# Optimization experiments

Measured on AMD Instinct MI355X. Metric: run time of the kernel, lower is better.

The kernel has to match this reference:

```python
import jax, jax.numpy as jnp
import numpy as np

N, E, DIN, H, HEADS = 50000, 800000, 128, 64, 4


def setup_inputs() -> dict:
    key = jax.random.key(0)
    ks = jax.random.split(key, 12)

    def p(k, shape, fan_in):
        return jax.random.normal(k, shape, dtype=jnp.float32) / np.float32(np.sqrt(fan_in))

    return dict(
        x=jax.random.normal(ks[0], (N, DIN), dtype=jnp.float32),
        edge_index=jax.random.randint(ks[1], (2, E), 0, N, dtype=jnp.int32),
        # GCNConv(input_dim, hidden)
        W_gcn=p(ks[2], (DIN, H), DIN), b_gcn=jnp.zeros((H,), jnp.float32),
        # GATConv(hidden, hidden, heads=4, concat=True)
        W_gat=p(ks[3], (H, HEADS * H), H),
        att_src=p(ks[4], (HEADS, H), H), att_dst=p(ks[5], (HEADS, H), H),
        b_gat=jnp.zeros((HEADS * H,), jnp.float32),
        # SAGEConv(4*hidden, hidden): lin_l (neighbors, with bias), lin_r (root, no bias)
        W_sage_l=p(ks[6], (HEADS * H, H), HEADS * H), b_sage=jnp.zeros((H,), jnp.float32),
        W_sage_r=p(ks[7], (HEADS * H, H), HEADS * H),
        # edge-pair MLP: Linear(2*hidden, hidden) -> ReLU -> Linear(hidden, 1)
        W1=p(ks[8], (2 * H, H), 2 * H), b1=jnp.zeros((H,), jnp.float32),
        W2=p(ks[9], (H, 1), H), b2=jnp.zeros((1,), jnp.float32),
    )


def reference(x, edge_index, W_gcn, b_gcn, W_gat, att_src, att_dst, b_gat,
              W_sage_l, b_sage, W_sage_r, W1, b1, W2, b2):
    n = x.shape[0]
    src, dst = edge_index[0], edge_index[1]
    loop = jnp.arange(n, dtype=edge_index.dtype)
    # edges with self-loops appended (GCN and GAT add self-loops by default)
    s2 = jnp.concatenate([src, loop])
    d2 = jnp.concatenate([dst, loop])

    h = x @ W_gcn                                            # [N, H]
    deg = jax.ops.segment_sum(jnp.ones_like(d2, jnp.float32), d2, num_segments=n)
    dinv = jnp.where(deg > 0, jax.lax.rsqrt(jnp.maximum(deg, 1e-12)), 0.0)
    norm = dinv[s2] * dinv[d2]                               # [E+N]
    h = jax.ops.segment_sum(h[s2] * norm[:, None], d2, num_segments=n) + b_gcn
    h = jax.nn.relu(h)                                       # dropout: identity in eval

    # ---- GATConv (heads=4, concat=True, negative_slope=0.2) ----
    g = (h @ W_gat).reshape(n, HEADS, H)                     # [N, heads, C]
    a_s = jnp.sum(g * att_src, axis=-1)                      # [N, heads]
    a_d = jnp.sum(g * att_dst, axis=-1)
    e = jax.nn.leaky_relu(a_s[s2] + a_d[d2], 0.2)            # [E+N, heads]
    m = jax.ops.segment_max(e, d2, num_segments=n)           # per-target max (stable softmax)
    e = jnp.exp(e - m[d2])
    z = jax.ops.segment_sum(e, d2, num_segments=n)
    alpha = e / (z[d2] + 1e-16)                              # edge softmax over incoming edges
    g = jax.ops.segment_sum(g[s2] * alpha[:, :, None], d2, num_segments=n)
    g = jax.nn.relu(g.reshape(n, HEADS * H) + b_gat)

    # ---- SAGEConv (mean aggregation, root weight, no self-loops) ----
    nsum = jax.ops.segment_sum(g[src], dst, num_segments=n)
    cnt = jax.ops.segment_sum(jnp.ones_like(dst, jnp.float32), dst, num_segments=n)
    mean = nsum / jnp.maximum(cnt, 1.0)[:, None]
    s = jax.nn.relu(mean @ W_sage_l + b_sage + g @ W_sage_r)  # [N, H]

    # ---- edge-pair MLP + sigmoid ----
    ef = jnp.concatenate([s[src], s[dst]], axis=1)            # [E, 2H]
    pred = jax.nn.relu(ef @ W1 + b1) @ W2 + b2                # [E, 1]
    return jax.nn.sigmoid(pred[:, 0])
```

## Files before the change

kernel.cpp:

```cpp
#include <hip/hip_runtime.h>
#include <math.h>

typedef float v2f __attribute__((ext_vector_type(2)));
static __device__ __forceinline__ float4 f4s(float v){ return make_float4(v,v,v,v); }
static __device__ __forceinline__ float4 f4add(float4 a, float4 b){ return make_float4(a.x+b.x,a.y+b.y,a.z+b.z,a.w+b.w); }
static __device__ __forceinline__ float4 f4max(float4 a, float4 b){ return make_float4(fmaxf(a.x,b.x),fmaxf(a.y,b.y),fmaxf(a.z,b.z),fmaxf(a.w,b.w)); }
static __device__ __forceinline__ float4 f4scale(float4 a, float s){ return make_float4(a.x*s,a.y*s,a.z*s,a.w*s); }
static __device__ __forceinline__ float4 f4fma(float4 acc, float s, float4 b){
  acc.x += s*b.x; acc.y += s*b.y; acc.z += s*b.z; acc.w += s*b.w; return acc;
}
static __device__ __forceinline__ float4 f4relu(float4 a){ return f4max(a, f4s(0.f)); }
static __device__ __forceinline__ float4 f4leaky(float4 a){
  return make_float4(a.x>0.f?a.x:0.2f*a.x, a.y>0.f?a.y:0.2f*a.y, a.z>0.f?a.z:0.2f*a.z, a.w>0.f?a.w:0.2f*a.w);
}
static __device__ __forceinline__ float4 f4expf(float4 a){ return make_float4(__expf(a.x),__expf(a.y),__expf(a.z),__expf(a.w)); }
static __device__ __forceinline__ unsigned short f2bf(float f){
  unsigned int u = __float_as_uint(f);
  unsigned int r = (u + 0x7fffu + ((u >> 16) & 1u)) >> 16;
  return (unsigned short)r;
}
static __device__ __forceinline__ ushort4 f2bf4(float4 f){
  ushort4 r; r.x=f2bf(f.x); r.y=f2bf(f.y); r.z=f2bf(f.z); r.w=f2bf(f.w); return r;
}
static __device__ __forceinline__ float4 bfu2f4(uint2 u){
  return make_float4(__uint_as_float(u.x << 16), __uint_as_float(u.x & 0xffff0000u),
                     __uint_as_float(u.y << 16), __uint_as_float(u.y & 0xffff0000u));
}
static __device__ __forceinline__ float4 bfu2f4_lo(uint4 u){ return bfu2f4(make_uint2(u.x, u.y)); }
static __device__ __forceinline__ float4 bfu2f4_hi(uint4 u){ return bfu2f4(make_uint2(u.z, u.w)); }

typedef __attribute__((ext_vector_type(8))) unsigned short u16x8;
static __device__ __forceinline__ u16x8 f2bf8(float4 a, float4 b){
  u16x8 r;
  r[0]=f2bf(a.x); r[1]=f2bf(a.y); r[2]=f2bf(a.z); r[3]=f2bf(a.w);
  r[4]=f2bf(b.x); r[5]=f2bf(b.y); r[6]=f2bf(b.z); r[7]=f2bf(b.w);
  return r;
}
static __device__ __forceinline__ void red2(float4& a, float4& b){
  a.x += __shfl_xor(a.x, 8); a.y += __shfl_xor(a.y, 8);
  a.z += __shfl_xor(a.z, 8); a.w += __shfl_xor(a.w, 8);
  b.x += __shfl_xor(b.x, 8); b.y += __shfl_xor(b.y, 8);
  b.z += __shfl_xor(b.z, 8); b.w += __shfl_xor(b.w, 8);
}
static __device__ __forceinline__ unsigned char f2fp8(float v){
  return (unsigned char)(__builtin_amdgcn_cvt_pk_fp8_f32(v, v, 0, false) & 0xff);
}
static __device__ __forceinline__ unsigned int f4_fp8x4(float4 v){
  unsigned int r = __builtin_amdgcn_cvt_pk_fp8_f32(v.x, v.y, 0, false);
  r = __builtin_amdgcn_cvt_pk_fp8_f32(v.z, v.w, r, true);
  return r;
}
static __device__ __forceinline__ float4 fp8x4_f4(unsigned int q){
  v2f lo = __builtin_amdgcn_cvt_pk_f32_fp8(q, false);
  v2f hi = __builtin_amdgcn_cvt_pk_f32_fp8(q, true);
  return make_float4(lo[0], lo[1], hi[0], hi[1]);
}

typedef __attribute__((ext_vector_type(8))) short bf16x8;
typedef __attribute__((ext_vector_type(4))) float f32x4;

__global__ __launch_bounds__(256) void k_rank(const int* __restrict__ dst, int* __restrict__ cnt,
                                              int* __restrict__ rank, int E){
  int t = blockIdx.x*256 + threadIdx.x;
  if (t < E) rank[t] = atomicAdd(&cnt[dst[t]], 1);
}
__global__ __launch_bounds__(256) void k_scan1(const int* __restrict__ cnt, int* __restrict__ excl,
                                               int* __restrict__ bsum, int n){
  __shared__ int sc[256];
  int t = threadIdx.x; int i = blockIdx.x*256 + t;
  int v = (i<n)?cnt[i]:0;
  sc[t]=v; __syncthreads();
  for (int o=1;o<256;o<<=1){ int a=(t>=o)?sc[t-o]:0; __syncthreads(); sc[t]+=a; __syncthreads(); }
  if (i<n) excl[i] = sc[t]-v;
  if (t==255) bsum[blockIdx.x] = sc[t];
}
__global__ __launch_bounds__(256) void k_scan2v(int* __restrict__ bsum, int nb,
                                                const float* __restrict__ Wg, const float* __restrict__ as,
                                                const float* __restrict__ ad, float* __restrict__ Vs,
                                                float* __restrict__ Vd){
  __shared__ int sc[256];
  int t = threadIdx.x;
  int v = (t<nb)?bsum[t]:0;
  sc[t]=v; __syncthreads();
  for (int o=1;o<256;o<<=1){ int a=(t>=o)?sc[t-o]:0; __syncthreads(); sc[t]+=a; __syncthreads(); }
  if (t<nb) bsum[t] = sc[t]-v;
  int h = t >> 6, k = t & 63;
  float s = 0.f, d = 0.f;
  const float* wr = Wg + (size_t)k*256 + h*64;
  const float* ar = as + h*64;
  const float* dr = ad + h*64;
  for (int c = 0; c < 64; ++c){ float w = wr[c]; s += w*ar[c]; d += w*dr[c]; }
  Vs[t] = s; Vd[t] = d;
}
__global__ __launch_bounds__(256) void k_scan3(const int* __restrict__ cnt, const int* __restrict__ excl,
                                               const int* __restrict__ bsum, int* __restrict__ offs,
                                               float* __restrict__ dinv, int n, int E){
  int i = blockIdx.x*256 + threadIdx.x;
  if (i < n){
    int o = excl[i] + bsum[blockIdx.x];
    offs[i] = o;
    dinv[i] = rsqrtf((float)cnt[i] + 1.0f);
    if (i == 0) offs[n] = E;
  }
}
__global__ __launch_bounds__(256) void k_fill(const int* __restrict__ src, const int* __restrict__ dst,
                                              const int* __restrict__ offs, const int* __restrict__ rank,
                                              int* __restrict__ csr, int E){
  int t = blockIdx.x*256 + threadIdx.x;
  if (t < E) csr[offs[dst[t]] + rank[t]] = src[t];
}

__global__ __launch_bounds__(256) void k_asdh(const unsigned short* __restrict__ Hh,
                                              const float* __restrict__ Vs, const float* __restrict__ Vd,
                                              float* __restrict__ D, int n){
  __shared__ float vs[256], vd[256];
  int t = threadIdx.x;
  vs[t] = Vs[t]; vd[t] = Vd[t];
  __syncthreads();
  int idx = blockIdx.x*256 + t;
  if (idx >= n*4) return;
  int nd = idx >> 2, h = idx & 3;
  const unsigned short* hr = Hh + (size_t)nd*64;
  const float* vsr = vs + h*64;
  const float* vdr = vd + h*64;
  float s = 0.f, d = 0.f;
  #pragma unroll
  for (int k = 0; k < 8; ++k){
    uint4 u = *(const uint4*)(hr + k*8);
    float4 lo = bfu2f4_lo(u), hi = bfu2f4_hi(u);
    const float* a = vsr + k*8;
    const float* b = vdr + k*8;
    s += lo.x*a[0]+lo.y*a[1]+lo.z*a[2]+lo.w*a[3] + hi.x*a[4]+hi.y*a[5]+hi.z*a[6]+hi.w*a[7];
    d += lo.x*b[0]+lo.y*b[1]+lo.z*b[2]+lo.w*b[3] + hi.x*b[4]+hi.y*b[5]+hi.z*b[6]+hi.w*b[7];
  }
  D[(size_t)nd*8 + h]     = s;
  D[(size_t)nd*8 + 4 + h] = d;
}

template<int K, int Cout, bool IBF16, bool SCALE, bool DUAL, bool H4, bool BRELU, bool OB16, bool O8>
__global__ __launch_bounds__(256) void k_mgemm(const void* __restrict__ in, int ldin,
                                               const float* __restrict__ Wa, int ldwa,
                                               const float* __restrict__ Wb, int ldwb,
                                               unsigned short* __restrict__ out,
                                               unsigned char* __restrict__ out8, int ldout,
                                               int n, const float* __restrict__ rowscale,
                                               const float* __restrict__ bias){
  constexpr int CC = Cout >> 4;
  constexpr int KB = K >> 5;
  constexpr int NH = H4 ? 4 : 1;
  extern __shared__ unsigned short wb[];
  int tid = threadIdx.x;
  constexpr int nslots = KB*CC*64;
  for (int s = tid; s < nslots; s += 256){
    int l = s & 63;
    int f = s >> 6;
    int cc = f % CC, kb = f / CC;
    int c  = cc*16 + (l & 15);
    int kr = kb*32 + ((l >> 4) << 3);
    const float* wp; int ld;
    if (DUAL && c >= (Cout/2)){ wp = Wb + (size_t)kr*ldwb + (c - Cout/2); ld = ldwb; }
    else                      { wp = Wa + (size_t)kr*ldwa + c;            ld = ldwa; }
    unsigned short* dp = &wb[s*8];
    #pragma unroll
    for (int j = 0; j < 8; ++j) dp[j] = f2bf(wp[(size_t)j*ld]);
  }
  __syncthreads();
  int wv = tid >> 6, l = tid & 63;
  int lrow = l & 15;
  int lk = (l >> 4) << 3;
  int ngrp = (n + 63) >> 6;
  const unsigned short* inb = (const unsigned short*)in;
  const float* inf = (const float*)in;
  for (int g = blockIdx.x; g < ngrp; g += gridDim.x){
    int r0 = (g << 6) + (wv << 4);
    int m = r0 + lrow;
    bf16x8 afr[NH][KB];
    #pragma unroll
    for (int h = 0; h < NH; ++h){
      #pragma unroll
      for (int kb = 0; kb < KB; ++kb){
        bf16x8 a = {0,0,0,0,0,0,0,0};
        if (m < n){
          int off = (H4 ? h*64 : 0) + kb*32 + lk;
          if (IBF16){
            a = *(const bf16x8*)(inb + (size_t)m*ldin + off);
          } else {
            const float* p = inf + (size_t)m*ldin + off;
            float4 f0 = *(const float4*)p;
            float4 f1 = *(const float4*)(p + 4);
            a[0]=(short)f2bf(f0.x); a[1]=(short)f2bf(f0.y); a[2]=(short)f2bf(f0.z); a[3]=(short)f2bf(f0.w);
            a[4]=(short)f2bf(f1.x); a[5]=(short)f2bf(f1.y); a[6]=(short)f2bf(f1.z); a[7]=(short)f2bf(f1.w);
          }
        }
        afr[h][kb] = a;
      }
    }
    int rbase = r0 + ((l >> 4) << 2);
    float sc[4];
    if (SCALE){
      #pragma unroll
      for (int r = 0; r < 4; ++r) sc[r] = (rbase + r < n) ? rowscale[rbase + r] : 0.f;
    }
    #pragma unroll
    for (int cc = 0; cc < CC; ++cc){
      f32x4 acc = {0.f, 0.f, 0.f, 0.f};
      constexpr int hstep = H4 ? 1 : 0;
      int hh = hstep ? (cc >> 2) : 0;
      #pragma unroll
      for (int kb = 0; kb < KB; ++kb){
        bf16x8 b = *(const bf16x8*)&wb[((kb*CC + cc)*64 + l)*8];
        acc = __builtin_amdgcn_mfma_f32_16x16x32_bf16(afr[hh][kb], b, acc, 0, 0, 0);
      }
      int c = cc*16 + lrow;
      float bv = BRELU ? bias[c] : 0.f;
      #pragma unroll
      for (int r = 0; r < 4; ++r){
        int rr = rbase + r;
        if (rr < n){
          float v = acc[r];
          if (SCALE) v *= sc[r];
          if (BRELU) v = fmaxf(v + bv, 0.f);
          if (OB16) out[(size_t)rr*ldout + c] = f2bf(v);
          if (O8)   out8[(size_t)rr*ldout + c] = f2fp8(v);
        }
      }
    }
  }
}

__global__ __launch_bounds__(256) void k_gcn(const unsigned char* __restrict__ a8, const float* __restrict__ dinv,
                                             const float* __restrict__ b, const int* __restrict__ offs,
                                             const int* __restrict__ csr, unsigned short* __restrict__ h,
                                             unsigned char* __restrict__ h8, int n){
  int l = threadIdx.x & 63;
  int node = (((blockIdx.x*256 + threadIdx.x) >> 6) << 2) + (l >> 4);
  int l15 = l & 15;
  int grp = l15 >> 3, sub = l15 & 7;
  bool ok = node < n;
  int beg = 0, end = 0;
  float di = 0.f;
  if (ok){ beg = offs[node]; end = offs[node+1]; di = dinv[node]; }
  float4 aL0 = f4s(0.f), aH0 = f4s(0.f), aL1 = f4s(0.f), aH1 = f4s(0.f);
  int i = beg + grp;
  for (; i + 2 < end; i += 4){
    int s0 = csr[i], s1 = csr[i+2];
    uint2 u0 = *(const uint2*)(a8 + (size_t)s0*64 + (sub<<3));
    uint2 u1 = *(const uint2*)(a8 + (size_t)s1*64 + (sub<<3));
    aL0 = f4add(aL0, fp8x4_f4(u0.x)); aH0 = f4add(aH0, fp8x4_f4(u0.y));
    aL1 = f4add(aL1, fp8x4_f4(u1.x)); aH1 = f4add(aH1, fp8x4_f4(u1.y));
  }
  if (i < end){
    int s0 = csr[i];
    uint2 u0 = *(const uint2*)(a8 + (size_t)s0*64 + (sub<<3));
    aL0 = f4add(aL0, fp8x4_f4(u0.x)); aH0 = f4add(aH0, fp8x4_f4(u0.y));
  }
  float4 aL = f4add(aL0, aL1), aH = f4add(aH0, aH1);
  red2(aL, aH);
  if (ok && grp == 0){
    uint2 us = *(const uint2*)(a8 + (size_t)node*64 + (sub<<3));
    aL = f4add(aL, fp8x4_f4(us.x)); aH = f4add(aH, fp8x4_f4(us.y));
    float4 b0 = *(const float4*)(b + (sub<<3));
    float4 b1 = *(const float4*)(b + (sub<<3) + 4);
    float4 r0 = f4relu(f4fma(b0, di, aL));
    float4 r1 = f4relu(f4fma(b1, di, aH));
    *(u16x8*)(h + (size_t)node*64 + (sub<<3)) = f2bf8(r0, r1);
    uint2 q; q.x = f4_fp8x4(r0); q.y = f4_fp8x4(r1);
    *(uint2*)(h8 + (size_t)node*64 + (sub<<3)) = q;
  }
}

#define GAT_CAP 128
__global__ __launch_bounds__(256) void k_gat2(const float* __restrict__ D, const unsigned char* __restrict__ H8,
                                              const int* __restrict__ offs, const int* __restrict__ csr,
                                              unsigned short* __restrict__ Y, int n){
  __shared__ float wl[8][GAT_CAP*4];
  __shared__ int   sl[8][GAT_CAP];
  int hw = threadIdx.x >> 5;
  int node = (blockIdx.x*256 + threadIdx.x) >> 5;
  int l5 = threadIdx.x & 31;
  if (node >= n) return;
  int beg = offs[node], end = offs[node+1];
  int deg = end - beg;
  float4 ed  = *(const float4*)(D + (size_t)node*8 + 4);
  float4 es0 = *(const float4*)(D + (size_t)node*8);
  float4 wself = f4expf(f4leaky(f4add(es0, ed)));
  float4 z4 = f4s(0.f);
  for (int i = beg + l5; i < end; i += 32){
    int s = csr[i];
    float4 w = f4expf(f4leaky(f4add(*(const float4*)(D + (size_t)s*8), ed)));
    int li = i - beg;
    if (li < GAT_CAP){ *(float4*)&wl[hw][li<<2] = w; sl[hw][li] = s << 6; }
    z4 = f4add(z4, w);
  }
  for (int m = 1; m < 32; m <<= 1){
    z4.x += __shfl_xor(z4.x, m); z4.y += __shfl_xor(z4.y, m);
    z4.z += __shfl_xor(z4.z, m); z4.w += __shfl_xor(z4.w, m);
  }
  z4 = f4add(z4, wself);
  int grp = l5 >> 4;
  int sub = l5 & 15;
  int c0b = sub << 2;
  float4 a0 = f4s(0.f), a1 = f4s(0.f), a2 = f4s(0.f), a3 = f4s(0.f);
  int nl = deg < GAT_CAP ? deg : GAT_CAP;
  int i = grp;
  for (; i + 2 < nl; i += 4){
    int o0 = sl[hw][i], o1 = sl[hw][i+2];
    float4 w0 = *(const float4*)&wl[hw][i<<2];
    float4 w1 = *(const float4*)&wl[hw][(i+2)<<2];
    unsigned int q0 = *(const unsigned int*)(H8 + o0 + c0b);
    unsigned int q1 = *(const unsigned int*)(H8 + o1 + c0b);
    float4 f0 = fp8x4_f4(q0);
    float4 f1 = fp8x4_f4(q1);
    a0 = f4fma(a0, w0.x, f0); a1 = f4fma(a1, w0.y, f0);
    a2 = f4fma(a2, w0.z, f0); a3 = f4fma(a3, w0.w, f0);
    a0 = f4fma(a0, w1.x, f1); a1 = f4fma(a1, w1.y, f1);
    a2 = f4fma(a2, w1.z, f1); a3 = f4fma(a3, w1.w, f1);
  }
  if (i < nl){
    float4 w0 = *(const float4*)&wl[hw][i<<2];
    float4 f0 = fp8x4_f4(*(const unsigned int*)(H8 + sl[hw][i] + c0b));
    a0 = f4fma(a0, w0.x, f0); a1 = f4fma(a1, w0.y, f0);
    a2 = f4fma(a2, w0.z, f0); a3 = f4fma(a3, w0.w, f0);
  }
  for (int j = nl + grp; j < deg; j += 2){
    int s = csr[beg+j];
    float4 e = f4leaky(f4add(*(const float4*)(D + (size_t)s*8), ed));
    float4 w = f4expf(e);
    float4 f0 = fp8x4_f4(*(const unsigned int*)(H8 + ((size_t)s << 6) + c0b));
    a0 = f4fma(a0, w.x, f0); a1 = f4fma(a1, w.y, f0);
    a2 = f4fma(a2, w.z, f0); a3 = f4fma(a3, w.w, f0);
  }
  a0.x += __shfl_xor(a0.x, 16); a0.y += __shfl_xor(a0.y, 16); a0.z += __shfl_xor(a0.z, 16); a0.w += __shfl_xor(a0.w, 16);
  a1.x += __shfl_xor(a1.x, 16); a1.y += __shfl_xor(a1.y, 16); a1.z += __shfl_xor(a1.z, 16); a1.w += __shfl_xor(a1.w, 16);
  a2.x += __shfl_xor(a2.x, 16); a2.y += __shfl_xor(a2.y, 16); a2.z += __shfl_xor(a2.z, 16); a2.w += __shfl_xor(a2.w, 16);
  a3.x += __shfl_xor(a3.x, 16); a3.y += __shfl_xor(a3.y, 16); a3.z += __shfl_xor(a3.z, 16); a3.w += __shfl_xor(a3.w, 16);
  if (grp == 0){
    float4 fs = fp8x4_f4(*(const unsigned int*)(H8 + ((size_t)node << 6) + c0b));
    a0 = f4fma(a0, wself.x, fs);
    a1 = f4fma(a1, wself.y, fs);
    a2 = f4fma(a2, wself.z, fs);
    a3 = f4fma(a3, wself.w, fs);
    a0 = f4scale(a0, 1.f/(z4.x + 1e-16f));
    a1 = f4scale(a1, 1.f/(z4.y + 1e-16f));
    a2 = f4scale(a2, 1.f/(z4.z + 1e-16f));
    a3 = f4scale(a3, 1.f/(z4.w + 1e-16f));
    unsigned short* yp = Y + (size_t)node*256 + (sub << 2);
    *(ushort4*)(yp)       = f2bf4(a0);
    *(ushort4*)(yp + 64)  = f2bf4(a1);
    *(ushort4*)(yp + 128) = f2bf4(a2);
    *(ushort4*)(yp + 192) = f2bf4(a3);
  }
}

__global__ __launch_bounds__(256) void k_sage(const unsigned char* __restrict__ T8, const unsigned short* __restrict__ T,
                                              const float* __restrict__ b, const int* __restrict__ offs,
                                              const int* __restrict__ csr, unsigned short* __restrict__ S, int n){
  int l = threadIdx.x & 63;
  int node = (((blockIdx.x*256 + threadIdx.x) >> 6) << 2) + (l >> 4);
  int l15 = l & 15;
  int grp = l15 >> 3, sub = l15 & 7;
  bool ok = node < n;
  int beg = 0, end = 0;
  if (ok){ beg = offs[node]; end = offs[node+1]; }
  float4 aL0 = f4s(0.f), aH0 = f4s(0.f), aL1 = f4s(0.f), aH1 = f4s(0.f);
  int i = beg + grp;
  for (; i + 2 < end; i += 4){
    int s0 = csr[i], s1 = csr[i+2];
    uint2 u0 = *(const uint2*)(T8 + (size_t)s0*128 + (sub<<3));
    uint2 u1 = *(const uint2*)(T8 + (size_t)s1*128 + (sub<<3));
    aL0 = f4add(aL0, fp8x4_f4(u0.x)); aH0 = f4add(aH0, fp8x4_f4(u0.y));
    aL1 = f4add(aL1, fp8x4_f4(u1.x)); aH1 = f4add(aH1, fp8x4_f4(u1.y));
  }
  if (i < end){
    int s0 = csr[i];
    uint2 u0 = *(const uint2*)(T8 + (size_t)s0*128 + (sub<<3));
    aL0 = f4add(aL0, fp8x4_f4(u0.x)); aH0 = f4add(aH0, fp8x4_f4(u0.y));
  }
  float4 aL = f4add(aL0, aL1), aH = f4add(aH0, aH1);
  red2(aL, aH);
  if (ok && grp == 0){
    float minv = 1.f / fmaxf((float)(end - beg), 1.f);
    uint4 ur = *(const uint4*)(T + (size_t)node*128 + 64 + (sub<<3));
    float4 b0 = *(const float4*)(b + (sub<<3));
    float4 b1 = *(const float4*)(b + (sub<<3) + 4);
    float4 r0 = f4relu(f4add(f4fma(b0, minv, aL), bfu2f4_lo(ur)));
    float4 r1 = f4relu(f4add(f4fma(b1, minv, aH), bfu2f4_hi(ur)));
    *(u16x8*)(S + (size_t)node*64 + (sub<<3)) = f2bf8(r0, r1);
  }
}

__global__ __launch_bounds__(256) void k_mlp(const unsigned char* __restrict__ T2,
                                             const float* __restrict__ b1, const float* __restrict__ W2,
                                             const float* __restrict__ b2, const int* __restrict__ src,
                                             const int* __restrict__ dst, float* __restrict__ out, int E){
  int t = threadIdx.x;
  int e = blockIdx.x*32 + (t >> 3);
  if (e >= E) return;
  int sub = t & 7;
  int s = src[e], d = dst[e];
  uint2 uu = *(const uint2*)(T2 + (size_t)s*128 + (sub<<3));
  uint2 vv = *(const uint2*)(T2 + (size_t)d*128 + 64 + (sub<<3));
  float4 u0 = fp8x4_f4(uu.x), u1 = fp8x4_f4(uu.y);
  float4 v0 = fp8x4_f4(vv.x), v1 = fp8x4_f4(vv.y);
  float4 bb0 = *(const float4*)(b1 + (sub<<3));
  float4 bb1 = *(const float4*)(b1 + (sub<<3) + 4);
  float4 w0 = *(const float4*)(W2 + (sub<<3));
  float4 w1 = *(const float4*)(W2 + (sub<<3) + 4);
  float4 ta = f4relu(f4add(f4add(u0, v0), bb0));
  float4 tb = f4relu(f4add(f4add(u1, v1), bb1));
  float p = ta.x*w0.x + ta.y*w0.y + ta.z*w0.z + ta.w*w0.w
          + tb.x*w1.x + tb.y*w1.y + tb.z*w1.z + tb.w*w1.w;
  p += __shfl_xor(p, 1);
  p += __shfl_xor(p, 2);
  p += __shfl_xor(p, 4);
  if (sub == 0) out[e] = 1.f / (1.f + __expf(-(p + b2[0])));
}

extern "C" void kernel_launch(void* const* d_in, const int* in_sizes, int n_in,
                              void* d_out, int out_size, void* d_ws, size_t ws_size,
                              hipStream_t stream){
  const float* x     = (const float*)d_in[0];
  const int*   eidx  = (const int*)  d_in[1];
  const float* W_gcn = (const float*)d_in[2];
  const float* b_gcn = (const float*)d_in[3];
  const float* W_gat = (const float*)d_in[4];
  const float* att_s = (const float*)d_in[5];
  const float* att_d = (const float*)d_in[6];
  const float* b_gat = (const float*)d_in[7];
  const float* W_sl  = (const float*)d_in[8];
  const float* b_sg  = (const float*)d_in[9];
  const float* W_sr  = (const float*)d_in[10];
  const float* W1    = (const float*)d_in[11];
  const float* b1    = (const float*)d_in[12];
  const float* W2    = (const float*)d_in[13];
  const float* b2    = (const float*)d_in[14];
  float* out = (float*)d_out;

  const int N = in_sizes[0] / 128;
  const int E = in_sizes[1] / 2;
  const int* src = eidx;
  const int* dst = eidx + E;

  float* ws   = (float*)d_ws;
  float* dinv = ws;
  float* D    = dinv + (size_t)N;
  float* Vs   = D + (size_t)N*8;
  float* Vd   = Vs + 256;
  unsigned short* A0 = (unsigned short*)(Vd + 256);
  unsigned short* H  = A0 + (size_t)N*64;
  unsigned short* Y  = H  + (size_t)N*64;
  unsigned short* G  = Y  + (size_t)N*256;
  unsigned short* T  = G  + (size_t)N*256;
  unsigned short* S  = T  + (size_t)N*128;
  unsigned char*  A8 = (unsigned char*)(S + (size_t)N*64);
  unsigned char*  H8 = A8 + (size_t)N*64;
  unsigned char*  T8 = H8 + (size_t)N*64;
  unsigned char*  T2 = T8 + (size_t)N*128;
  int* cnt  = (int*)(T2 + (size_t)N*128);
  int* excl = cnt + N;
  int* bsum = excl + N;
  int* offs = bsum + 256;
  int* rank = offs + N + 1;
  int* csr  = rank + E;

  const int nb = (N + 255) / 256;
  const int gtiles = (N + 63) / 64;
  const int nwb = (N + 15) / 16;

  hipMemsetAsync(cnt, 0, (size_t)N*sizeof(int), stream);
  k_rank<<<(E+255)/256, 256, 0, stream>>>(dst, cnt, rank, E);
  k_scan1<<<nb, 256, 0, stream>>>(cnt, excl, bsum, N);
  k_scan2v<<<1, 256, 0, stream>>>(bsum, nb, W_gat, att_s, att_d, Vs, Vd);
  k_scan3<<<nb, 256, 0, stream>>>(cnt, excl, bsum, offs, dinv, N, E);
  k_fill<<<(E+255)/256, 256, 0, stream>>>(src, dst, offs, rank, csr, E);

  k_mgemm<128, 64, false, true, false, false, false, false, true><<<gtiles, 256, 128*64*2, stream>>>(
      x, 128, W_gcn, 64, nullptr, 0, nullptr, A8, 64, N, dinv, nullptr);
  k_gcn <<<nwb, 256, 0, stream>>>(A8, dinv, b_gcn, offs, csr, H, H8, N);
  k_asdh<<<(N*4+255)/256, 256, 0, stream>>>(H, Vs, Vd, D, N);

  k_gat2<<<(N+7)/8, 256, 0, stream>>>(D, H8, offs, csr, Y, N);
  k_mgemm<64, 256, true, false, false, true, true, true, false><<<gtiles, 256, 64*256*2, stream>>>(
      Y, 256, W_gat, 256, nullptr, 0, G, nullptr, 256, N, nullptr, b_gat);

  k_mgemm<256, 128, true, false, true, false, false, true, true><<<gtiles, 256, 256*128*2, stream>>>(
      G, 256, W_sl, 64, W_sr, 64, T, T8, 128, N, nullptr, nullptr);
  k_sage<<<nwb, 256, 0, stream>>>(T8, T, b_sg, offs, csr, S, N);

  k_mgemm<64, 128, true, false, true, false, false, false, true><<<gtiles, 256, 64*128*2, stream>>>(
      S, 64, W1, 64, W1 + 64*64, 64, nullptr, T2, 128, N, nullptr, nullptr);
  k_mlp <<<(E+31)/32, 256, 0, stream>>>(T2, b1, W2, b2, src, dst, out, E);
}
```

Baseline: 323.2 us.

## Fuse GAT and SAGE GEMMs into one persistent kernel; fold attention dots into GCN

The two back-to-back GEMMs (GAT output projection with bias and ReLU, then the SAGE dual projection) become one persistent kernel. It keeps the intermediate 256-wide G tile in LDS instead of writing and re-reading it from global memory, and stages both weight matrices once per block. The per-node attention dot products (the former k_asdh) move into the GCN aggregation kernel, which removes a launch and the bf16 H buffer. SAGE now reads only the 64-wide fp8 neighbour projection and a separate bf16 root buffer. The cost is a large LDS footprint that limits occupancy, and a fixed grid of 256 blocks.

```diff
diff --git a/kernel.cpp b/kernel.cpp
--- a/kernel.cpp
+++ b/kernel.cpp
@@ -54,6 +54,9 @@
   v2f lo = __builtin_amdgcn_cvt_pk_f32_fp8(q, false);
   v2f hi = __builtin_amdgcn_cvt_pk_f32_fp8(q, true);
   return make_float4(lo[0], lo[1], hi[0], hi[1]);
+}
+static __device__ __forceinline__ float dot8(float4 a, float4 b, const float* v){
+  return a.x*v[0]+a.y*v[1]+a.z*v[2]+a.w*v[3]+b.x*v[4]+b.y*v[5]+b.z*v[6]+b.w*v[7];
 }
 
 typedef __attribute__((ext_vector_type(8))) short bf16x8;
@@ -108,33 +111,6 @@
                                               int* __restrict__ csr, int E){
   int t = blockIdx.x*256 + threadIdx.x;
   if (t < E) csr[offs[dst[t]] + rank[t]] = src[t];
-}
-
-__global__ __launch_bounds__(256) void k_asdh(const unsigned short* __restrict__ Hh,
-                                              const float* __restrict__ Vs, const float* __restrict__ Vd,
-                                              float* __restrict__ D, int n){
-  __shared__ float vs[256], vd[256];
-  int t = threadIdx.x;
-  vs[t] = Vs[t]; vd[t] = Vd[t];
-  __syncthreads();
-  int idx = blockIdx.x*256 + t;
-  if (idx >= n*4) return;
-  int nd = idx >> 2, h = idx & 3;
-  const unsigned short* hr = Hh + (size_t)nd*64;
-  const float* vsr = vs + h*64;
-  const float* vdr = vd + h*64;
-  float s = 0.f, d = 0.f;
-  #pragma unroll
-  for (int k = 0; k < 8; ++k){
-    uint4 u = *(const uint4*)(hr + k*8);
-    float4 lo = bfu2f4_lo(u), hi = bfu2f4_hi(u);
-    const float* a = vsr + k*8;
-    const float* b = vdr + k*8;
-    s += lo.x*a[0]+lo.y*a[1]+lo.z*a[2]+lo.w*a[3] + hi.x*a[4]+hi.y*a[5]+hi.z*a[6]+hi.w*a[7];
-    d += lo.x*b[0]+lo.y*b[1]+lo.z*b[2]+lo.w*b[3] + hi.x*b[4]+hi.y*b[5]+hi.z*b[6]+hi.w*b[7];
-  }
-  D[(size_t)nd*8 + h]     = s;
-  D[(size_t)nd*8 + 4 + h] = d;
 }
 
 template<int K, int Cout, bool IBF16, bool SCALE, bool DUAL, bool H4, bool BRELU, bool OB16, bool O8>
@@ -228,10 +204,110 @@
   }
 }
 
+__global__ __launch_bounds__(256) void k_gatsage(const unsigned short* __restrict__ Y,
+                                                 const float* __restrict__ Wg,
+                                                 const float* __restrict__ bg,
+                                                 const float* __restrict__ Wl,
+                                                 const float* __restrict__ Wr,
+                                                 unsigned short* __restrict__ R,
+                                                 unsigned char* __restrict__ P8, int n){
+  constexpr int LDG = 264;
+  extern __shared__ unsigned short lds[];
+  unsigned short* wb1 = lds;
+  unsigned short* wb2 = wb1 + 2048*8;
+  unsigned short* gb  = wb2 + 4096*8;
+  int tid = threadIdx.x;
+  for (int s = tid; s < 2048; s += 256){
+    int l = s & 63, f = s >> 6;
+    int cc = f & 15, kb = f >> 4;
+    int c  = cc*16 + (l & 15);
+    int kr = kb*32 + ((l >> 4) << 3);
+    const float* wp = Wg + (size_t)kr*256 + c;
+    unsigned short* dp = &wb1[s*8];
+    #pragma unroll
+    for (int j = 0; j < 8; ++j) dp[j] = f2bf(wp[(size_t)j*256]);
+  }
+  for (int s = tid; s < 4096; s += 256){
+    int l = s & 63, f = s >> 6;
+    int cc = f & 7, kb = f >> 3;
+    int c  = cc*16 + (l & 15);
+    int kr = kb*32 + ((l >> 4) << 3);
+    const float* wp = (c >= 64) ? (Wr + (size_t)kr*64 + (c - 64)) : (Wl + (size_t)kr*64 + c);
+    unsigned short* dp = &wb2[s*8];
+    #pragma unroll
+    for (int j = 0; j < 8; ++j) dp[j] = f2bf(wp[(size_t)j*64]);
+  }
+  __syncthreads();
+  int wv = tid >> 6, l = tid & 63;
+  int lrow = l & 15;
+  int lk = (l >> 4) << 3;
+  int rbase4 = (l >> 4) << 2;
+  int ngrp = (n + 63) >> 6;
+  for (int g = blockIdx.x; g < ngrp; g += gridDim.x){
+    int r0 = (g << 6) + (wv << 4);
+    int m = r0 + lrow;
+    bf16x8 afr[4][2];
+    #pragma unroll
+    for (int h = 0; h < 4; ++h){
+      #pragma unroll
+      for (int kb = 0; kb < 2; ++kb){
+        bf16x8 a = {0,0,0,0,0,0,0,0};
+        if (m < n) a = *(const bf16x8*)(Y + (size_t)m*256 + h*64 + kb*32 + lk);
+        afr[h][kb] = a;
+      }
+    }
+    #pragma unroll
+    for (int cc = 0; cc < 16; ++cc){
+      f32x4 acc = {0.f, 0.f, 0.f, 0.f};
+      int hh = cc >> 2;
+      #pragma unroll
+      for (int kb = 0; kb < 2; ++kb){
+        bf16x8 b = *(const bf16x8*)&wb1[((kb*16 + cc)*64 + l)*8];
+        acc = __builtin_amdgcn_mfma_f32_16x16x32_bf16(afr[hh][kb], b, acc, 0, 0, 0);
+      }
+      int c = cc*16 + lrow;
+      float bv = bg[c];
+      #pragma unroll
+      for (int r = 0; r < 4; ++r){
+        int lr = (wv << 4) + rbase4 + r;
+        gb[lr*LDG + c] = f2bf(fmaxf(acc[r] + bv, 0.f));
+      }
+    }
+    bf16x8 afb[8];
+    #pragma unroll
+    for (int kb = 0; kb < 8; ++kb)
+      afb[kb] = *(const bf16x8*)&gb[((wv << 4) + lrow)*LDG + kb*32 + lk];
+    #pragma unroll
+    for (int cc = 0; cc < 8; ++cc){
+      f32x4 acc = {0.f, 0.f, 0.f, 0.f};
+      #pragma unroll
+      for (int kb = 0; kb < 8; ++kb){
+        bf16x8 b = *(const bf16x8*)&wb2[((kb*8 + cc)*64 + l)*8];
+        acc = __builtin_amdgcn_mfma_f32_16x16x32_bf16(afb[kb], b, acc, 0, 0, 0);
+      }
+      int c = cc*16 + lrow;
+      #pragma unroll
+      for (int r = 0; r < 4; ++r){
+        int rr = r0 + rbase4 + r;
+        if (rr < n){
+          float v = acc[r];
+          if (c < 64) P8[(size_t)rr*64 + c] = f2fp8(v);
+          else        R[(size_t)rr*64 + (c - 64)] = f2bf(v);
+        }
+      }
+    }
+  }
+}
+
 __global__ __launch_bounds__(256) void k_gcn(const unsigned char* __restrict__ a8, const float* __restrict__ dinv,
                                              const float* __restrict__ b, const int* __restrict__ offs,
-                                             const int* __restrict__ csr, unsigned short* __restrict__ h,
-                                             unsigned char* __restrict__ h8, int n){
+                                             const int* __restrict__ csr, const float* __restrict__ Vs,
+                                             const float* __restrict__ Vd, unsigned char* __restrict__ h8,
+                                             float* __restrict__ D, int n){
+  __shared__ float svs[256], svd[256];
+  svs[threadIdx.x] = Vs[threadIdx.x];
+  svd[threadIdx.x] = Vd[threadIdx.x];
+  __syncthreads();
   int l = threadIdx.x & 63;
   int node = (((blockIdx.x*256 + threadIdx.x) >> 6) << 2) + (l >> 4);
   int l15 = l & 15;
@@ -256,16 +332,32 @@
   }
   float4 aL = f4add(aL0, aL1), aH = f4add(aH0, aH1);
   red2(aL, aH);
-  if (ok && grp == 0){
+  if (ok){
     uint2 us = *(const uint2*)(a8 + (size_t)node*64 + (sub<<3));
     aL = f4add(aL, fp8x4_f4(us.x)); aH = f4add(aH, fp8x4_f4(us.y));
     float4 b0 = *(const float4*)(b + (sub<<3));
     float4 b1 = *(const float4*)(b + (sub<<3) + 4);
     float4 r0 = f4relu(f4fma(b0, di, aL));
     float4 r1 = f4relu(f4fma(b1, di, aH));
-    *(u16x8*)(h + (size_t)node*64 + (sub<<3)) = f2bf8(r0, r1);
-    uint2 q; q.x = f4_fp8x4(r0); q.y = f4_fp8x4(r1);
-    *(uint2*)(h8 + (size_t)node*64 + (sub<<3)) = q;
+    if (grp == 0){
+      uint2 q; q.x = f4_fp8x4(r0); q.y = f4_fp8x4(r1);
+      *(uint2*)(h8 + (size_t)node*64 + (sub<<3)) = q;
+    }
+    const float* vs0 = svs + (grp*128) + (sub<<3);
+    const float* vd0 = svd + (grp*128) + (sub<<3);
+    float s0 = dot8(r0, r1, vs0);
+    float s1 = dot8(r0, r1, vs0 + 64);
+    float d0 = dot8(r0, r1, vd0);
+    float d1 = dot8(r0, r1, vd0 + 64);
+    #pragma unroll
+    for (int o = 1; o < 8; o <<= 1){
+      s0 += __shfl_xor(s0, o); s1 += __shfl_xor(s1, o);
+      d0 += __shfl_xor(d0, o); d1 += __shfl_xor(d1, o);
+    }
+    if (sub == 0){
+      *(float2*)(D + (size_t)node*8 + grp*2)     = make_float2(s0, s1);
+      *(float2*)(D + (size_t)node*8 + 4 + grp*2) = make_float2(d0, d1);
+    }
   }
 }
 
@@ -352,7 +444,7 @@
   }
 }
 
-__global__ __launch_bounds__(256) void k_sage(const unsigned char* __restrict__ T8, const unsigned short* __restrict__ T,
+__global__ __launch_bounds__(256) void k_sage(const unsigned char* __restrict__ P8, const unsigned short* __restrict__ R,
                                               const float* __restrict__ b, const int* __restrict__ offs,
                                               const int* __restrict__ csr, unsigned short* __restrict__ S, int n){
   int l = threadIdx.x & 63;
@@ -366,21 +458,21 @@
   int i = beg + grp;
   for (; i + 2 < end; i += 4){
     int s0 = csr[i], s1 = csr[i+2];
-    uint2 u0 = *(const uint2*)(T8 + (size_t)s0*128 + (sub<<3));
-    uint2 u1 = *(const uint2*)(T8 + (size_t)s1*128 + (sub<<3));
+    uint2 u0 = *(const uint2*)(P8 + (size_t)s0*64 + (sub<<3));
+    uint2 u1 = *(const uint2*)(P8 + (size_t)s1*64 + (sub<<3));
     aL0 = f4add(aL0, fp8x4_f4(u0.x)); aH0 = f4add(aH0, fp8x4_f4(u0.y));
     aL1 = f4add(aL1, fp8x4_f4(u1.x)); aH1 = f4add(aH1, fp8x4_f4(u1.y));
   }
   if (i < end){
     int s0 = csr[i];
-    uint2 u0 = *(const uint2*)(T8 + (size_t)s0*128 + (sub<<3));
+    uint2 u0 = *(const uint2*)(P8 + (size_t)s0*64 + (sub<<3));
     aL0 = f4add(aL0, fp8x4_f4(u0.x)); aH0 = f4add(aH0, fp8x4_f4(u0.y));
   }
   float4 aL = f4add(aL0, aL1), aH = f4add(aH0, aH1);
   red2(aL, aH);
   if (ok && grp == 0){
     float minv = 1.f / fmaxf((float)(end - beg), 1.f);
-    uint4 ur = *(const uint4*)(T + (size_t)node*128 + 64 + (sub<<3));
+    uint4 ur = *(const uint4*)(R + (size_t)node*64 + (sub<<3));
     float4 b0 = *(const float4*)(b + (sub<<3));
     float4 b1 = *(const float4*)(b + (sub<<3) + 4);
     float4 r0 = f4relu(f4add(f4fma(b0, minv, aL), bfu2f4_lo(ur)));
@@ -446,16 +538,13 @@
   float* D    = dinv + (size_t)N;
   float* Vs   = D + (size_t)N*8;
   float* Vd   = Vs + 256;
-  unsigned short* A0 = (unsigned short*)(Vd + 256);
-  unsigned short* H  = A0 + (size_t)N*64;
-  unsigned short* Y  = H  + (size_t)N*64;
-  unsigned short* G  = Y  + (size_t)N*256;
-  unsigned short* T  = G  + (size_t)N*256;
-  unsigned short* S  = T  + (size_t)N*128;
+  unsigned short* Y  = (unsigned short*)(Vd + 256);
+  unsigned short* R  = Y + (size_t)N*256;
+  unsigned short* S  = R + (size_t)N*64;
   unsigned char*  A8 = (unsigned char*)(S + (size_t)N*64);
   unsigned char*  H8 = A8 + (size_t)N*64;
-  unsigned char*  T8 = H8 + (size_t)N*64;
-  unsigned char*  T2 = T8 + (size_t)N*128;
+  unsigned char*  P8 = H8 + (size_t)N*64;
+  unsigned char*  T2 = P8 + (size_t)N*64;
   int* cnt  = (int*)(T2 + (size_t)N*128);
   int* excl = cnt + N;
   int* bsum = excl + N;
@@ -466,6 +555,13 @@
   const int nb = (N + 255) / 256;
   const int gtiles = (N + 63) / 64;
   const int nwb = (N + 15) / 16;
+  const int GSH = (2048*8 + 4096*8 + 64*264) * 2;
+
+  static bool s_attr = false;
+  if (!s_attr){
+    hipFuncSetAttribute((const void*)k_gatsage, hipFuncAttributeMaxDynamicSharedMemorySize, GSH);
+    s_attr = true;
+  }
 
   hipMemsetAsync(cnt, 0, (size_t)N*sizeof(int), stream);
   k_rank<<<(E+255)/256, 256, 0, stream>>>(dst, cnt, rank, E);
@@ -476,16 +572,13 @@
 
   k_mgemm<128, 64, false, true, false, false, false, false, true><<<gtiles, 256, 128*64*2, stream>>>(
       x, 128, W_gcn, 64, nullptr, 0, nullptr, A8, 64, N, dinv, nullptr);
-  k_gcn <<<nwb, 256, 0, stream>>>(A8, dinv, b_gcn, offs, csr, H, H8, N);
-  k_asdh<<<(N*4+255)/256, 256, 0, stream>>>(H, Vs, Vd, D, N);
+  k_gcn <<<nwb, 256, 0, stream>>>(A8, dinv, b_gcn, offs, csr, Vs, Vd, H8, D, N);
 
   k_gat2<<<(N+7)/8, 256, 0, stream>>>(D, H8, offs, csr, Y, N);
-  k_mgemm<64, 256, true, false, false, true, true, true, false><<<gtiles, 256, 64*256*2, stream>>>(
-      Y, 256, W_gat, 256, nullptr, 0, G, nullptr, 256, N, nullptr, b_gat);
-
-  k_mgemm<256, 128, true, false, true, false, false, true, true><<<gtiles, 256, 256*128*2, stream>>>(
-      G, 256, W_sl, 64, W_sr, 64, T, T8, 128, N, nullptr, nullptr);
-  k_sage<<<nwb, 256, 0, stream>>>(T8, T, b_sg, offs, csr, S, N);
+
+  k_gatsage<<<256, 256, GSH, stream>>>(Y, W_gat, b_gat, W_sl, W_sr, R, P8, N);
+
+  k_sage<<<nwb, 256, 0, stream>>>(P8, R, b_sg, offs, csr, S, N);
 
   k_mgemm<64, 128, true, false, true, false, false, false, true><<<gtiles, 256, 64*128*2, stream>>>(
       S, 64, W1, 64, W1 + 64*64, 64, nullptr, T2, 128, N, nullptr, nullptr);
```

Measured after the change: 291.0 us. 10.0% less time.
